# Kernel optimization log

Hardware: AMD Instinct MI355X
Metric: run time of the kernel (lower is better)

Reference implementation:

```python
import jax, jax.numpy as jnp
import numpy as np

B, I, H = 256, 512, 512


def _lin_init(k, out_dim, in_dim):
    bound = 1.0 / np.sqrt(in_dim)
    kw, kb = jax.random.split(k)
    W = jax.random.uniform(kw, (out_dim, in_dim), minval=-bound, maxval=bound, dtype=jnp.float32)
    b = jax.random.uniform(kb, (out_dim,), minval=-bound, maxval=bound, dtype=jnp.float32)
    return W, b


def setup_inputs() -> dict:
    key = jax.random.key(0)
    ks = jax.random.split(key, 16)
    inp = {}
    inp['inputs'] = jax.random.normal(ks[0], (B, I), dtype=jnp.float32)
    inp['h0'] = jax.random.normal(ks[1], (B, H), dtype=jnp.float32) * 0.1
    inp['c0'] = jax.random.normal(ks[2], (B, H), dtype=jnp.float32) * 0.1
    inp['hebb'] = jax.random.uniform(ks[3], (B, H, H), minval=-0.01, maxval=0.01, dtype=jnp.float32)
    # plastic recurrent weights: w = 0.02*rand - 0.01, alpha = 1e-4*rand
    inp['w'] = 0.02 * jax.random.uniform(ks[4], (H, H), dtype=jnp.float32) - 0.01
    inp['alpha'] = 1e-4 * jax.random.uniform(ks[5], (1, 1, H), dtype=jnp.float32)
    inp['Wxf'], inp['bxf'] = _lin_init(ks[6], H, I)
    inp['Whf'], inp['bhf'] = _lin_init(ks[7], H, H)
    inp['Wxi'], inp['bxi'] = _lin_init(ks[8], H, I)
    inp['Whi'], inp['bhi'] = _lin_init(ks[9], H, H)
    inp['Wxo'], inp['bxo'] = _lin_init(ks[10], H, I)
    inp['Who'], inp['bho'] = _lin_init(ks[11], H, H)
    inp['Wxc'], inp['bxc'] = _lin_init(ks[12], H, I)
    inp['Wmod'], inp['bmod'] = _lin_init(ks[13], 1, H)   # h2mod: H -> 1
    inp['Wfan'], inp['bfan'] = _lin_init(ks[14], H, 1)   # modfanout: 1 -> H
    return inp


def reference(inputs, h0, c0, hebb, w, alpha,
              Wxf, bxf, Whf, bhf, Wxi, bxi, Whi, bhi,
              Wxo, bxo, Who, bho, Wxc, bxc, Wmod, bmod, Wfan, bfan):
    # gates (torch Linear: y = x @ W.T + b)
    fgt = jax.nn.sigmoid(inputs @ Wxf.T + bxf + h0 @ Whf.T + bhf)
    ipt = jax.nn.sigmoid(inputs @ Wxi.T + bxi + h0 @ Whi.T + bhi)
    opt = jax.nn.sigmoid(inputs @ Wxo.T + bxo + h0 @ Who.T + bho)
    # plastic recurrent path: h0 @ (w + alpha * hebb), per-sample fast weights
    h2c = jnp.einsum('bh,bhk->bk', h0, w + alpha * hebb)
    inputstocell = jnp.tanh(inputs @ Wxc.T + bxc + h2c)
    cell = fgt * c0 + ipt * inputstocell
    hactiv = opt * jnp.tanh(cell)
    # Hebbian outer-product trace update with neuromodulated learning rate
    deltahebb = jnp.einsum('bh,bk->bhk', h0, inputstocell)  # [B,H,H]
    myeta = jnp.tanh(hactiv @ Wmod.T + bmod)                # [B,1]
    myeta = myeta * Wfan[:, 0][None, :] + bfan              # modfanout(1->H): [B,H]
    hebb_new = jnp.clip(hebb + myeta[:, None, :] * deltahebb, -2.0, 2.0)
    return hactiv, cell, hebb_new
```

## Files before the change

kernel.cpp:

```cpp
#include <hip/hip_runtime.h>
#include <hip/hip_bf16.h>
#include <math.h>

#define B_ 256
#define I_ 512
#define H_ 512
#define BH (B_*H_)
#define KA 1024
#define NCH 8
#define HCH (H_/NCH)

typedef float f4v  __attribute__((ext_vector_type(4)));
typedef short s8v  __attribute__((ext_vector_type(8)));
typedef float f32x4 __attribute__((ext_vector_type(4)));


#define A_ELEMS (256*1024)
#define B_ELEMS (2048*1024)

__global__ __launch_bounds__(256) void k_convert(
    const float* __restrict__ inputs, const float* __restrict__ h0,
    const float* __restrict__ Wxf, const float* __restrict__ Whf,
    const float* __restrict__ Wxi, const float* __restrict__ Whi,
    const float* __restrict__ Wxo, const float* __restrict__ Who,
    const float* __restrict__ Wxc, const float* __restrict__ w,
    ushort* __restrict__ Ahi, ushort* __restrict__ Alo,
    ushort* __restrict__ Bhi, ushort* __restrict__ Blo) {
    const int NTOT = A_ELEMS + B_ELEMS;
    int stride = gridDim.x * blockDim.x;
    for (int f = blockIdx.x * blockDim.x + threadIdx.x; f < NTOT; f += stride) {
        float x; ushort* dhi; ushort* dlo; int idx;
        if (f < A_ELEMS) {
            idx = f;
            int m = f >> 10, k = f & 1023;
            x = (k < 512) ? inputs[m * 512 + k] : h0[m * 512 + (k - 512)];
            dhi = Ahi; dlo = Alo;
        } else {
            idx = f - A_ELEMS;
            int n = idx >> 10, k = idx & 1023;
            int g = n >> 9, ko = n & 511;
            if (k < 512) {
                const float* W = (g == 0) ? Wxf : (g == 1) ? Wxi : (g == 2) ? Wxo : Wxc;
                x = W[ko * 512 + k];
            } else if (g < 3) {
                const float* W = (g == 0) ? Whf : (g == 1) ? Whi : Who;
                x = W[ko * 512 + (k - 512)];
            } else {
                x = w[(size_t)(k - 512) * 512 + ko];
            }
            dhi = Bhi; dlo = Blo;
        }
        __hip_bfloat16 h = __float2bfloat16(x);
        float hf = __bfloat162float(h);
        __hip_bfloat16 l = __float2bfloat16(x - hf);
        dhi[idx] = *(ushort*)&h;
        dlo[idx] = *(ushort*)&l;
    }
}

__global__ __launch_bounds__(256) void k_mfma_gates(
    const ushort* __restrict__ Ahi, const ushort* __restrict__ Alo,
    const ushort* __restrict__ Bhi, const ushort* __restrict__ Blo,
    const float* __restrict__ bxf, const float* __restrict__ bhf,
    const float* __restrict__ bxi, const float* __restrict__ bhi,
    const float* __restrict__ bxo, const float* __restrict__ bho,
    const float* __restrict__ bxc,
    float* __restrict__ pre) {
    int wave = threadIdx.x >> 6, lane = threadIdx.x & 63;
    int tile = blockIdx.x * 4 + wave;
    int m0 = (tile & 15) << 4;
    int n0 = (tile >> 4) << 4;
    int r  = lane & 15;
    int kg = lane >> 4;

    const s8v* pa_hi = (const s8v*)(Ahi + (size_t)(m0 + r) * KA + kg * 8);
    const s8v* pa_lo = (const s8v*)(Alo + (size_t)(m0 + r) * KA + kg * 8);
    const s8v* pb_hi = (const s8v*)(Bhi + (size_t)(n0 + r) * KA + kg * 8);
    const s8v* pb_lo = (const s8v*)(Blo + (size_t)(n0 + r) * KA + kg * 8);

    f32x4 acc = {0.f, 0.f, 0.f, 0.f};
    #pragma unroll 4
    for (int kc = 0; kc < 32; ++kc) {
        s8v ah = pa_hi[kc * 4];
        s8v al = pa_lo[kc * 4];
        s8v bh = pb_hi[kc * 4];
        s8v bl = pb_lo[kc * 4];
        acc = __builtin_amdgcn_mfma_f32_16x16x32_bf16(ah, bh, acc, 0, 0, 0);
        acc = __builtin_amdgcn_mfma_f32_16x16x32_bf16(ah, bl, acc, 0, 0, 0);
        acc = __builtin_amdgcn_mfma_f32_16x16x32_bf16(al, bh, acc, 0, 0, 0);
    }

    int g  = n0 >> 9;
    int ko = (n0 & 511) + r;
    float bias;
    if (g == 0)      bias = bxf[ko] + bhf[ko];
    else if (g == 1) bias = bxi[ko] + bhi[ko];
    else if (g == 2) bias = bxo[ko] + bho[ko];
    else             bias = bxc[ko];
    #pragma unroll
    for (int j = 0; j < 4; ++j) {
        int m = m0 + kg * 4 + j;
        pre[(size_t)g * BH + (size_t)m * H_ + ko] = acc[j] + bias;
    }
}

__global__ __launch_bounds__(256) void k_hebbdot(
    const float* __restrict__ hebb, const float* __restrict__ h0,
    float* __restrict__ part) {
    __shared__ float h0s[HCH];
    __shared__ float4 red[256];
    int hbid = blockIdx.x;
    int b  = hbid >> 3;
    int ch = hbid & 7;
    int tid = threadIdx.x;

    if (tid < HCH) h0s[tid] = h0[b * H_ + ch * HCH + tid];
    __syncthreads();

    const float4* hbp = (const float4*)(hebb + ((size_t)b * H_ + (size_t)ch * HCH) * H_);
    int tk = tid & 127;
    int th = tid >> 7;
    float4 acc = make_float4(0.f, 0.f, 0.f, 0.f);
    #pragma unroll 8
    for (int r = 0; r < 32; ++r) {
        int hh = th * 32 + r;
        float s = h0s[hh];
        float4 vv = hbp[(size_t)hh * 128 + tk];
        acc.x += s * vv.x; acc.y += s * vv.y;
        acc.z += s * vv.z; acc.w += s * vv.w;
    }
    red[tid] = acc;
    __syncthreads();
    if (tid < 128) {
        float4 a = red[tid], c = red[tid + 128];
        float4 o = make_float4(a.x + c.x, a.y + c.y, a.z + c.z, a.w + c.w);
        ((float4*)(part + ((size_t)ch * B_ + b) * H_))[tid] = o;
    }
}

__global__ __launch_bounds__(256) void k_finalize(
    const float* __restrict__ pre, const float* __restrict__ part,
    const float* __restrict__ c0, const float* __restrict__ alpha,
    const float* __restrict__ Wmod, const float* __restrict__ bmod,
    const float* __restrict__ Wfan, const float* __restrict__ bfan,
    float* __restrict__ out, float* __restrict__ v) {

    int b = blockIdx.x;
    int t = threadIdx.x;

    float c2r[2];
    float local = 0.f;
    #pragma unroll
    for (int s = 0; s < 2; ++s) {
        int k = t + s * 256;
        float dot = 0.f;
        #pragma unroll
        for (int c = 0; c < NCH; ++c) dot += part[((size_t)c * B_ + b) * H_ + k];
        size_t off = (size_t)b * H_ + k;
        float pf = pre[0 * BH + off];
        float pi = pre[1 * BH + off];
        float po = pre[2 * BH + off];
        float pc = pre[3 * BH + off];
        float c2 = tanhf(pc + alpha[k] * dot);
        float fg = 1.f / (1.f + expf(-pf));
        float ig = 1.f / (1.f + expf(-pi));
        float og = 1.f / (1.f + expf(-po));
        float cell = fg * c0[off] + ig * c2;
        float ha = og * tanhf(cell);
        out[off] = ha;
        out[BH + off] = cell;
        c2r[s] = c2;
        local += ha * Wmod[k];
    }
    float x = local;
    #pragma unroll
    for (int o = 32; o > 0; o >>= 1) x += __shfl_down(x, o, 64);
    __shared__ float red[4];
    int wid = t >> 6, lane = t & 63;
    if (lane == 0) red[wid] = x;
    __syncthreads();
    float s4 = red[0] + red[1] + red[2] + red[3];
    float myeta = tanhf(s4 + bmod[0]);
    #pragma unroll
    for (int s = 0; s < 2; ++s) {
        int k = t + s * 256;
        size_t off = (size_t)b * H_ + k;
        v[off] = (myeta * Wfan[k] + bfan[k]) * c2r[s];
    }
}

__global__ __launch_bounds__(256) void k_update(
    const float4* __restrict__ hebb, const float* __restrict__ h0,
    const float* __restrict__ v, float* __restrict__ out) {
    const int total = B_ * H_ * (H_ / 4);
    int stride = gridDim.x * blockDim.x;
    int base = blockIdx.x * blockDim.x + threadIdx.x;
    for (int f = total - stride + base; f >= 0; f -= stride) {
        int k4 = f & 127;
        int h  = (f >> 7) & 511;
        int b  = f >> 16;
        float u = h0[(b << 9) + h];
        const float4* vv4 = (const float4*)v;
        float4 vv = vv4[(b << 7) + k4];
        float4 hb = hebb[f];
        f4v r;
        r.x = fminf(fmaxf(hb.x + u * vv.x, -2.f), 2.f);
        r.y = fminf(fmaxf(hb.y + u * vv.y, -2.f), 2.f);
        r.z = fminf(fmaxf(hb.z + u * vv.z, -2.f), 2.f);
        r.w = fminf(fmaxf(hb.w + u * vv.w, -2.f), 2.f);
        __builtin_nontemporal_store(r, (f4v*)(out) + f);
    }
}

extern "C" void kernel_launch(void* const* d_in, const int* in_sizes, int n_in,
                              void* d_out, int out_size, void* d_ws, size_t ws_size,
                              hipStream_t stream) {
    const float* inputs = (const float*)d_in[0];
    const float* h0     = (const float*)d_in[1];
    const float* c0     = (const float*)d_in[2];
    const float* hebb   = (const float*)d_in[3];
    const float* w      = (const float*)d_in[4];
    const float* alpha  = (const float*)d_in[5];
    const float* Wxf = (const float*)d_in[6];  const float* bxf = (const float*)d_in[7];
    const float* Whf = (const float*)d_in[8];  const float* bhf = (const float*)d_in[9];
    const float* Wxi = (const float*)d_in[10]; const float* bxi = (const float*)d_in[11];
    const float* Whi = (const float*)d_in[12]; const float* bhi = (const float*)d_in[13];
    const float* Wxo = (const float*)d_in[14]; const float* bxo = (const float*)d_in[15];
    const float* Who = (const float*)d_in[16]; const float* bho = (const float*)d_in[17];
    const float* Wxc = (const float*)d_in[18]; const float* bxc = (const float*)d_in[19];
    const float* Wmod = (const float*)d_in[20]; const float* bmod = (const float*)d_in[21];
    const float* Wfan = (const float*)d_in[22]; const float* bfan = (const float*)d_in[23];

    float* out = (float*)d_out;
    float* ws  = (float*)d_ws;
    float*  pre  = ws;
    float*  part = ws + 4 * BH;
    float*  vbuf = ws + 12 * BH;
    ushort* Ahi  = (ushort*)(ws + 13 * BH);
    ushort* Alo  = Ahi + A_ELEMS;
    ushort* Bhi  = Alo + A_ELEMS;
    ushort* Blo  = Bhi + B_ELEMS;

    k_convert<<<2048, 256, 0, stream>>>(inputs, h0,
        Wxf, Whf, Wxi, Whi, Wxo, Who, Wxc, w, Ahi, Alo, Bhi, Blo);
    k_mfma_gates<<<512, 256, 0, stream>>>(Ahi, Alo, Bhi, Blo,
        bxf, bhf, bxi, bhi, bxo, bho, bxc, pre);
    k_hebbdot<<<B_ * NCH, 256, 0, stream>>>(hebb, h0, part);
    k_finalize<<<B_, 256, 0, stream>>>(pre, part, c0, alpha,
                                       Wmod, bmod, Wfan, bfan, out, vbuf);
    k_update<<<2048, 256, 0, stream>>>((const float4*)hebb, h0, vbuf,
                                       out + 2 * BH);
}
```

Baseline: 188.2 us.

## Fuse bf16 split conversion into MFMA gate GEMM and merge with hebb dot

Removes the separate conversion kernel that wrote hi/lo bf16 copies of the activations and weights. The GEMM now loads fp32 operands directly and splits them into hi/lo bf16 in registers. That GEMM is also merged with the Hebbian dot-product kernel into one launch, with block ranges dispatched by block id. This cuts one full write and re-read of the operand staging buffers and two kernel launches, and lets the GEMM blocks overlap with the bandwidth-bound hebb reads. The cost is redundant conversion work across tiles and strided uncoalesced loads of w for the cell gate.

```diff
diff --git a/kernel.cpp b/kernel.cpp
--- a/kernel.cpp
+++ b/kernel.cpp
@@ -6,135 +6,127 @@
 #define I_ 512
 #define H_ 512
 #define BH (B_*H_)
-#define KA 1024
 #define NCH 8
 #define HCH (H_/NCH)
+#define NHEBB (B_*NCH)
+#define NGATE 512
 
 typedef float f4v  __attribute__((ext_vector_type(4)));
 typedef short s8v  __attribute__((ext_vector_type(8)));
 typedef float f32x4 __attribute__((ext_vector_type(4)));
 
 
-#define A_ELEMS (256*1024)
-#define B_ELEMS (2048*1024)
-
-__global__ __launch_bounds__(256) void k_convert(
-    const float* __restrict__ inputs, const float* __restrict__ h0,
+__global__ __launch_bounds__(256) void k_dot_gates(
+    const float* __restrict__ hebb, const float* __restrict__ h0,
+    const float* __restrict__ inputs,
     const float* __restrict__ Wxf, const float* __restrict__ Whf,
     const float* __restrict__ Wxi, const float* __restrict__ Whi,
     const float* __restrict__ Wxo, const float* __restrict__ Who,
     const float* __restrict__ Wxc, const float* __restrict__ w,
-    ushort* __restrict__ Ahi, ushort* __restrict__ Alo,
-    ushort* __restrict__ Bhi, ushort* __restrict__ Blo) {
-    const int NTOT = A_ELEMS + B_ELEMS;
-    int stride = gridDim.x * blockDim.x;
-    for (int f = blockIdx.x * blockDim.x + threadIdx.x; f < NTOT; f += stride) {
-        float x; ushort* dhi; ushort* dlo; int idx;
-        if (f < A_ELEMS) {
-            idx = f;
-            int m = f >> 10, k = f & 1023;
-            x = (k < 512) ? inputs[m * 512 + k] : h0[m * 512 + (k - 512)];
-            dhi = Ahi; dlo = Alo;
-        } else {
-            idx = f - A_ELEMS;
-            int n = idx >> 10, k = idx & 1023;
-            int g = n >> 9, ko = n & 511;
-            if (k < 512) {
-                const float* W = (g == 0) ? Wxf : (g == 1) ? Wxi : (g == 2) ? Wxo : Wxc;
-                x = W[ko * 512 + k];
-            } else if (g < 3) {
-                const float* W = (g == 0) ? Whf : (g == 1) ? Whi : Who;
-                x = W[ko * 512 + (k - 512)];
-            } else {
-                x = w[(size_t)(k - 512) * 512 + ko];
-            }
-            dhi = Bhi; dlo = Blo;
-        }
-        __hip_bfloat16 h = __float2bfloat16(x);
-        float hf = __bfloat162float(h);
-        __hip_bfloat16 l = __float2bfloat16(x - hf);
-        dhi[idx] = *(ushort*)&h;
-        dlo[idx] = *(ushort*)&l;
-    }
-}
-
-__global__ __launch_bounds__(256) void k_mfma_gates(
-    const ushort* __restrict__ Ahi, const ushort* __restrict__ Alo,
-    const ushort* __restrict__ Bhi, const ushort* __restrict__ Blo,
     const float* __restrict__ bxf, const float* __restrict__ bhf,
     const float* __restrict__ bxi, const float* __restrict__ bhi,
     const float* __restrict__ bxo, const float* __restrict__ bho,
     const float* __restrict__ bxc,
-    float* __restrict__ pre) {
-    int wave = threadIdx.x >> 6, lane = threadIdx.x & 63;
-    int tile = blockIdx.x * 4 + wave;
-    int m0 = (tile & 15) << 4;
-    int n0 = (tile >> 4) << 4;
-    int r  = lane & 15;
-    int kg = lane >> 4;
-
-    const s8v* pa_hi = (const s8v*)(Ahi + (size_t)(m0 + r) * KA + kg * 8);
-    const s8v* pa_lo = (const s8v*)(Alo + (size_t)(m0 + r) * KA + kg * 8);
-    const s8v* pb_hi = (const s8v*)(Bhi + (size_t)(n0 + r) * KA + kg * 8);
-    const s8v* pb_lo = (const s8v*)(Blo + (size_t)(n0 + r) * KA + kg * 8);
-
-    f32x4 acc = {0.f, 0.f, 0.f, 0.f};
-    #pragma unroll 4
-    for (int kc = 0; kc < 32; ++kc) {
-        s8v ah = pa_hi[kc * 4];
-        s8v al = pa_lo[kc * 4];
-        s8v bh = pb_hi[kc * 4];
-        s8v bl = pb_lo[kc * 4];
-        acc = __builtin_amdgcn_mfma_f32_16x16x32_bf16(ah, bh, acc, 0, 0, 0);
-        acc = __builtin_amdgcn_mfma_f32_16x16x32_bf16(ah, bl, acc, 0, 0, 0);
-        acc = __builtin_amdgcn_mfma_f32_16x16x32_bf16(al, bh, acc, 0, 0, 0);
-    }
-
-    int g  = n0 >> 9;
-    int ko = (n0 & 511) + r;
-    float bias;
-    if (g == 0)      bias = bxf[ko] + bhf[ko];
-    else if (g == 1) bias = bxi[ko] + bhi[ko];
-    else if (g == 2) bias = bxo[ko] + bho[ko];
-    else             bias = bxc[ko];
-    #pragma unroll
-    for (int j = 0; j < 4; ++j) {
-        int m = m0 + kg * 4 + j;
-        pre[(size_t)g * BH + (size_t)m * H_ + ko] = acc[j] + bias;
-    }
-}
-
-__global__ __launch_bounds__(256) void k_hebbdot(
-    const float* __restrict__ hebb, const float* __restrict__ h0,
-    float* __restrict__ part) {
-    __shared__ float h0s[HCH];
+    float* __restrict__ pre, float* __restrict__ part) {
+
+    __shared__ float  h0s[HCH];
     __shared__ float4 red[256];
-    int hbid = blockIdx.x;
-    int b  = hbid >> 3;
-    int ch = hbid & 7;
+    int bid = blockIdx.x;
     int tid = threadIdx.x;
 
-    if (tid < HCH) h0s[tid] = h0[b * H_ + ch * HCH + tid];
-    __syncthreads();
-
-    const float4* hbp = (const float4*)(hebb + ((size_t)b * H_ + (size_t)ch * HCH) * H_);
-    int tk = tid & 127;
-    int th = tid >> 7;
-    float4 acc = make_float4(0.f, 0.f, 0.f, 0.f);
-    #pragma unroll 8
-    for (int r = 0; r < 32; ++r) {
-        int hh = th * 32 + r;
-        float s = h0s[hh];
-        float4 vv = hbp[(size_t)hh * 128 + tk];
-        acc.x += s * vv.x; acc.y += s * vv.y;
-        acc.z += s * vv.z; acc.w += s * vv.w;
-    }
-    red[tid] = acc;
-    __syncthreads();
-    if (tid < 128) {
-        float4 a = red[tid], c = red[tid + 128];
-        float4 o = make_float4(a.x + c.x, a.y + c.y, a.z + c.z, a.w + c.w);
-        ((float4*)(part + ((size_t)ch * B_ + b) * H_))[tid] = o;
+    if (bid < NHEBB) {
+        int b  = bid >> 3;
+        int ch = bid & 7;
+        if (tid < HCH) h0s[tid] = h0[b * H_ + ch * HCH + tid];
+        __syncthreads();
+
+        const float4* hbp = (const float4*)(hebb + ((size_t)b * H_ + (size_t)ch * HCH) * H_);
+        int tk = tid & 127;
+        int th = tid >> 7;
+        float4 acc = make_float4(0.f, 0.f, 0.f, 0.f);
+        #pragma unroll 8
+        for (int r = 0; r < 32; ++r) {
+            int hh = th * 32 + r;
+            float s = h0s[hh];
+            float4 vv = hbp[(size_t)hh * 128 + tk];
+            acc.x += s * vv.x; acc.y += s * vv.y;
+            acc.z += s * vv.z; acc.w += s * vv.w;
+        }
+        red[tid] = acc;
+        __syncthreads();
+        if (tid < 128) {
+            float4 a = red[tid], c = red[tid + 128];
+            float4 o = make_float4(a.x + c.x, a.y + c.y, a.z + c.z, a.w + c.w);
+            ((float4*)(part + ((size_t)ch * B_ + b) * H_))[tid] = o;
+        }
+    } else {
+        int wave = tid >> 6, lane = tid & 63;
+        int tile = (bid - NHEBB) * 4 + wave;
+        int m0 = (tile & 15) << 4;
+        int n0 = (tile >> 4) << 4;
+        int r  = lane & 15;
+        int kg = lane >> 4;
+        int g  = n0 >> 9;
+        int ko0 = n0 & 511;
+        int ko  = ko0 + r;
+
+        const float* Wx  = (g == 0) ? Wxf : (g == 1) ? Wxi : (g == 2) ? Wxo : Wxc;
+        const float* Whp = (g == 0) ? Whf : (g == 1) ? Whi : Who;
+        const float* arow_i = inputs + (size_t)(m0 + r) * 512;
+        const float* arow_h = h0     + (size_t)(m0 + r) * 512;
+        const float* brow_x = Wx     + (size_t)ko * 512;
+        const float* brow_h = Whp    + (size_t)ko * 512;
+
+        f32x4 acc = {0.f, 0.f, 0.f, 0.f};
+        #pragma unroll 2
+        for (int kc = 0; kc < 32; ++kc) {
+            int kb = kc * 32 + kg * 8;
+            float a[8], bb[8];
+            if (kc < 16) {
+                *(float4*)&a[0]  = *(const float4*)&arow_i[kb];
+                *(float4*)&a[4]  = *(const float4*)&arow_i[kb + 4];
+                *(float4*)&bb[0] = *(const float4*)&brow_x[kb];
+                *(float4*)&bb[4] = *(const float4*)&brow_x[kb + 4];
+            } else {
+                int c = kb - 512;
+                *(float4*)&a[0] = *(const float4*)&arow_h[c];
+                *(float4*)&a[4] = *(const float4*)&arow_h[c + 4];
+                if (g < 3) {
+                    *(float4*)&bb[0] = *(const float4*)&brow_h[c];
+                    *(float4*)&bb[4] = *(const float4*)&brow_h[c + 4];
+                } else {
+                    #pragma unroll
+                    for (int j = 0; j < 8; ++j)
+                        bb[j] = w[(size_t)(c + j) * 512 + ko];
+                }
+            }
+            union { s8v v; ushort u[8]; } Ah, Al, Bh, Bl;
+            #pragma unroll
+            for (int j = 0; j < 8; ++j) {
+                __hip_bfloat16 hx = __float2bfloat16(a[j]);
+                float hxf = __bfloat162float(hx);
+                __hip_bfloat16 lx = __float2bfloat16(a[j] - hxf);
+                Ah.u[j] = *(ushort*)&hx; Al.u[j] = *(ushort*)&lx;
+                __hip_bfloat16 hy = __float2bfloat16(bb[j]);
+                float hyf = __bfloat162float(hy);
+                __hip_bfloat16 ly = __float2bfloat16(bb[j] - hyf);
+                Bh.u[j] = *(ushort*)&hy; Bl.u[j] = *(ushort*)&ly;
+            }
+            acc = __builtin_amdgcn_mfma_f32_16x16x32_bf16(Ah.v, Bh.v, acc, 0, 0, 0);
+            acc = __builtin_amdgcn_mfma_f32_16x16x32_bf16(Ah.v, Bl.v, acc, 0, 0, 0);
+            acc = __builtin_amdgcn_mfma_f32_16x16x32_bf16(Al.v, Bh.v, acc, 0, 0, 0);
+        }
+
+        float bias;
+        if (g == 0)      bias = bxf[ko] + bhf[ko];
+        else if (g == 1) bias = bxi[ko] + bhi[ko];
+        else if (g == 2) bias = bxo[ko] + bho[ko];
+        else             bias = bxc[ko];
+        #pragma unroll
+        for (int j = 0; j < 4; ++j) {
+            int m = m0 + kg * 4 + j;
+            pre[(size_t)g * BH + (size_t)m * H_ + ko] = acc[j] + bias;
+        }
     }
 }
 
@@ -233,19 +225,15 @@
 
     float* out = (float*)d_out;
     float* ws  = (float*)d_ws;
-    float*  pre  = ws;
-    float*  part = ws + 4 * BH;
-    float*  vbuf = ws + 12 * BH;
-    ushort* Ahi  = (ushort*)(ws + 13 * BH);
-    ushort* Alo  = Ahi + A_ELEMS;
-    ushort* Bhi  = Alo + A_ELEMS;
-    ushort* Blo  = Bhi + B_ELEMS;
-
-    k_convert<<<2048, 256, 0, stream>>>(inputs, h0,
-        Wxf, Whf, Wxi, Whi, Wxo, Who, Wxc, w, Ahi, Alo, Bhi, Blo);
-    k_mfma_gates<<<512, 256, 0, stream>>>(Ahi, Alo, Bhi, Blo,
-        bxf, bhf, bxi, bhi, bxo, bho, bxc, pre);
-    k_hebbdot<<<B_ * NCH, 256, 0, stream>>>(hebb, h0, part);
+    float* pre  = ws;
+    float* part = ws + 4 * BH;
+    float* vbuf = ws + 12 * BH;
+
+    k_dot_gates<<<NHEBB + NGATE, 256, 0, stream>>>(
+        hebb, h0, inputs,
+        Wxf, Whf, Wxi, Whi, Wxo, Who, Wxc, w,
+        bxf, bhf, bxi, bhi, bxo, bho, bxc,
+        pre, part);
     k_finalize<<<B_, 256, 0, stream>>>(pre, part, c0, alpha,
                                        Wmod, bmod, Wfan, bfan, out, vbuf);
     k_update<<<2048, 256, 0, stream>>>((const float4*)hebb, h0, vbuf,
```

Result: slower. 234.5 us (+24.6%).
